# Kernel optimization log

Measured on AMD Instinct MI355X. Metric: run time of the kernel, lower is better.

Reference implementation:

```python
import jax, jax.numpy as jnp
import numpy as np

UNITS = 1024
D_MODEL = 1024
H = 16
DK = 64
DV = 64
M = 128
B = 4
S = 1024


def setup_inputs() -> dict:
    key = jax.random.key(0)
    ks = jax.random.split(key, 12)
    s = 1.0 / np.sqrt(D_MODEL)
    inp = {
        "queries": jax.random.normal(ks[0], (B, S, D_MODEL), jnp.float32),
        "keys": jax.random.normal(ks[1], (B, S, D_MODEL), jnp.float32),
        "values": jax.random.normal(ks[2], (B, S, D_MODEL), jnp.float32),
        "Wq": jax.random.normal(ks[3], (D_MODEL, H * DK), jnp.float32) * s,
        "bq": jnp.zeros((H * DK,), jnp.float32),
        "Wk": jax.random.normal(ks[4], (D_MODEL, H * DK), jnp.float32) * s,
        "bk": jnp.zeros((H * DK,), jnp.float32),
        "Wv": jax.random.normal(ks[5], (D_MODEL, H * DV), jnp.float32) * s,
        "bv": jnp.zeros((H * DV,), jnp.float32),
        "Wo": jax.random.normal(ks[6], (H * DV, UNITS), jnp.float32) * (1.0 / np.sqrt(H * DV)),
        "bo": jnp.zeros((UNITS,), jnp.float32),
        "mk": jax.random.normal(ks[7], (1, M, H * DK), jnp.float32) * 0.1,
        "mv": jax.random.normal(ks[8], (1, M, H * DV), jnp.float32) * 0.1,
        "h": H,
    }
    return inp


def reference(queries, keys, values, Wq, bq, Wk, bk, Wv, bv, Wo, bo, mk, mv, h):
    Bq, Sq, _ = queries.shape
    m = mk.shape[1]
    dk = Wk.shape[1] // h
    dv = Wv.shape[1] // h
    scale_m = jnp.sqrt(jnp.asarray(m, queries.dtype))

    # Q projection: [B, h, Sq, dk]
    q = (queries @ Wq + bq).reshape(Bq, Sq, h, dk).transpose(0, 2, 1, 3)

    # K/V projections with m learned memory slots concatenated on the seq axis
    k_flat = jnp.concatenate(
        [keys @ Wk + bk, scale_m * jnp.broadcast_to(mk, (Bq, m, h * dk))], axis=1
    )  # [B, Sk+m, h*dk]
    v_flat = jnp.concatenate(
        [values @ Wv + bv, scale_m * jnp.broadcast_to(mv, (Bq, m, h * dv))], axis=1
    )  # [B, Sk+m, h*dv]
    Skm = k_flat.shape[1]
    k = k_flat.reshape(Bq, Skm, h, dk).transpose(0, 2, 1, 3)  # [B, h, Sk+m, dk]
    v = v_flat.reshape(Bq, Skm, h, dv).transpose(0, 2, 1, 3)  # [B, h, Sk+m, dv]

    # Scaled dot-product attention over sequence + memory slots
    scores = jnp.einsum("bhqd,bhkd->bhqk", q, k) / jnp.sqrt(jnp.asarray(dk, q.dtype))
    attn = jax.nn.softmax(scores, axis=-1)  # [B, h, Sq, Sk+m]
    out = jnp.einsum("bhqk,bhkd->bhqd", attn, v)  # [B, h, Sq, dv]
    out = out.transpose(0, 2, 1, 3).reshape(Bq, Sq, h * dv)
    return out @ Wo + bo
```

## Files before the change

kernel.cpp:

```cpp
#include <hip/hip_runtime.h>

typedef __attribute__((ext_vector_type(8))) __bf16 bf16x8;
typedef __attribute__((ext_vector_type(4))) float f32x4;

#define DEVINL __device__ __forceinline__

constexpr int BZ = 4;
constexpr int SEQ = 1024;
constexpr int DMODEL = 1024;
constexpr int NH = 16;
constexpr int HD = 64;
constexpr int MSLOT = 128;
constexpr int NT = BZ * SEQ;
constexpr int SKM = SEQ + MSLOT;
constexpr int VT_LD = BZ * SKM;
constexpr float SCALE_M = 11.313708498984761f;
constexpr float SCEXP = 0.18033688011112042f;
constexpr size_t OF_QIN  = 0;
constexpr size_t OF_KIN  = OF_QIN  + (size_t)NT * DMODEL;
constexpr size_t OF_VIN  = OF_KIN  + (size_t)NT * DMODEL;
constexpr size_t OF_WQT  = OF_VIN  + (size_t)NT * DMODEL;
constexpr size_t OF_WKT  = OF_WQT  + (size_t)DMODEL * DMODEL;
constexpr size_t OF_WVT  = OF_WKT  + (size_t)DMODEL * DMODEL;
constexpr size_t OF_WOT  = OF_WVT  + (size_t)DMODEL * DMODEL;
constexpr size_t OF_QB   = OF_WOT  + (size_t)DMODEL * DMODEL;
constexpr size_t OF_KPR  = OF_QB   + (size_t)NT * DMODEL;
constexpr size_t OF_KMEM = OF_KPR  + (size_t)NT * DMODEL;
constexpr size_t OF_VTG  = OF_KMEM + (size_t)MSLOT * DMODEL;
constexpr size_t OF_AOUT = OF_VTG  + (size_t)DMODEL * VT_LD;

DEVINL unsigned short f2bf(float f) {
  union { float f; unsigned u; } v; v.f = f;
  unsigned r = v.u + 0x7FFF + ((v.u >> 16) & 1);
  return (unsigned short)(r >> 16);
}

#if __has_builtin(__builtin_amdgcn_cvt_pk_bf16_f32)
DEVINL unsigned pack2(float a, float b) {
  auto t = __builtin_amdgcn_cvt_pk_bf16_f32(a, b);
  unsigned r; __builtin_memcpy(&r, &t, 4); return r;
}
#else
DEVINL unsigned pack2(float a, float b) {
  return (unsigned)f2bf(a) | ((unsigned)f2bf(b) << 16);
}
#endif

#if __has_builtin(__builtin_amdgcn_exp2f)
DEVINL float fast_exp2(float x) { return __builtin_amdgcn_exp2f(x); }
#else
DEVINL float fast_exp2(float x) { return exp2f(x); }
#endif

DEVINL f32x4 mfma16(bf16x8 a, bf16x8 b, f32x4 c) {
  return __builtin_amdgcn_mfma_f32_16x16x32_bf16(a, b, c, 0, 0, 0);
}

DEVINL void gload16(const unsigned short* gp, unsigned short* lp) {
  __builtin_amdgcn_global_load_lds(
      (const __attribute__((address_space(1))) unsigned int*)(const void*)gp,
      (__attribute__((address_space(3))) unsigned int*)(void*)lp, 16, 0, 0);
}

__global__ __launch_bounds__(256) void prep_all(
    const float* __restrict__ q, const float* __restrict__ k, const float* __restrict__ v,
    const float* __restrict__ W0, const float* __restrict__ W1,
    const float* __restrict__ W2, const float* __restrict__ W3,
    const float* __restrict__ mk, const float* __restrict__ mv,
    unsigned short* __restrict__ dq, unsigned short* __restrict__ dk,
    unsigned short* __restrict__ dv,
    unsigned short* __restrict__ d0, unsigned short* __restrict__ d1,
    unsigned short* __restrict__ d2, unsigned short* __restrict__ d3,
    unsigned short* __restrict__ Kmm, unsigned short* __restrict__ VtG) {
  __shared__ float t[32][65];
  const int tid = threadIdx.x;
  const int bid = blockIdx.x;
  if (bid < 6144) {
    const int tz = bid >> 11;
    const float* src = (tz == 0) ? q : (tz == 1) ? k : v;
    unsigned short* dst = (tz == 0) ? dq : (tz == 1) ? dk : dv;
    int i = ((bid & 2047) * 256 + tid) * 8;
    float4 v0 = *(const float4*)(src + i);
    float4 v1 = *(const float4*)(src + i + 4);
    union { unsigned u2[4]; uint4 v; } o;
    o.u2[0] = pack2(v0.x, v0.y); o.u2[1] = pack2(v0.z, v0.w);
    o.u2[2] = pack2(v1.x, v1.y); o.u2[3] = pack2(v1.z, v1.w);
    *(uint4*)(dst + i) = o.v;
  } else if (bid < 8192) {
    const int rel = bid - 6144;
    const int z = rel >> 9, rem = rel & 511;
    const float* src = (z == 0) ? W0 : (z == 1) ? W1 : (z == 2) ? W2 : W3;
    unsigned short* dst = (z == 0) ? d0 : (z == 1) ? d1 : (z == 2) ? d2 : d3;
    const int n0 = (rem & 31) * 32, k0 = (rem >> 5) * 64;
    {
      int c = tid & 31, rg = tid >> 5;
#pragma unroll
      for (int rr = 0; rr < 8; ++rr)
        t[c][rg * 8 + rr] = src[(size_t)(k0 + rg * 8 + rr) * DMODEL + n0 + c];
    }
    __syncthreads();
    {
      int n = tid >> 3, ck = tid & 7;
      union { unsigned short u[8]; uint4 v; } o;
#pragma unroll
      for (int j = 0; j < 8; ++j) o.u[j] = f2bf(t[n][ck * 8 + j]);
      *(uint4*)(dst + (size_t)(n0 + n) * DMODEL + k0 + ck * 8) = o.v;
    }
  } else if (bid < 8704) {
    int i = (bid - 8192) * 256 + tid;
    Kmm[i] = f2bf(mk[i] * SCALE_M);
  } else {
    const int rel = bid - 8704;
    const int j0 = (rel & 3) * 32, c0 = (rel >> 2) * 32;
    const int tx = tid & 31, ty = tid >> 5;
#pragma unroll
    for (int r = 0; r < 4; ++r)
      t[ty + r * 8][tx] = mv[(size_t)(j0 + ty + r * 8) * DMODEL + c0 + tx];
    __syncthreads();
#pragma unroll
    for (int r = 0; r < 4; ++r) {
      int c = c0 + ty + r * 8;
      unsigned short vv = f2bf(t[tx][ty + r * 8] * SCALE_M);
#pragma unroll
      for (int bb = 0; bb < BZ; ++bb)
        VtG[(size_t)c * VT_LD + bb * SKM + SEQ + j0 + tx] = vv;
    }
  }
}


DEVINL void gemm_stage(const unsigned short* big, const unsigned short* sm,
                       unsigned short* B0, unsigned short* B1,
                       unsigned short* S0, unsigned short* S1,
                       int k0, int tid) {
#pragma unroll
  for (int hb = 0; hb < 2; ++hb) {
    unsigned short* bl = hb ? B1 : B0;
#pragma unroll
    for (int gi = 0; gi < 2; ++gi) {
      int g = gi * 256 + tid;
      int row = g >> 2, slot = g & 3;
      gload16(big + (size_t)row * DMODEL + k0 + hb * 32 + slot * 8, bl + g * 8);
    }
    unsigned short* sl = hb ? S1 : S0;
    int row = tid >> 2, slot = tid & 3;
    gload16(sm + (size_t)row * DMODEL + k0 + hb * 32 + slot * 8, sl + tid * 8);
  }
}

DEVINL void gemm_compute(const unsigned short* B0, const unsigned short* B1,
                         const unsigned short* S0, const unsigned short* S1,
                         int wr, int wc, int quad, int l16, f32x4 acc[4][2]) {
#pragma unroll
  for (int hb = 0; hb < 2; ++hb) {
    const unsigned short* bl = hb ? B1 : B0;
    const unsigned short* sl = hb ? S1 : S0;
    bf16x8 af[4], bfr[2];
#pragma unroll
    for (int rb = 0; rb < 4; ++rb)
      af[rb] = *(const bf16x8*)(bl + (wr * 64 + rb * 16 + l16) * 32 + quad * 8);
#pragma unroll
    for (int cb = 0; cb < 2; ++cb)
      bfr[cb] = *(const bf16x8*)(sl + (wc * 32 + cb * 16 + l16) * 32 + quad * 8);
#pragma unroll
    for (int rb = 0; rb < 4; ++rb)
#pragma unroll
      for (int cb = 0; cb < 2; ++cb)
        acc[rb][cb] = mfma16(af[rb], bfr[cb], acc[rb][cb]);
  }
}

__global__ __launch_bounds__(256) void proj_qkv(
    const unsigned short* __restrict__ Qin, const unsigned short* __restrict__ Kin,
    const unsigned short* __restrict__ Vin, const unsigned short* __restrict__ Wqt,
    const unsigned short* __restrict__ Wkt, const unsigned short* __restrict__ Wvt,
    const float* __restrict__ bq, const float* __restrict__ bk,
    const float* __restrict__ bv, unsigned short* __restrict__ Qbp,
    unsigned short* __restrict__ Kprp, unsigned short* __restrict__ VtG) {
  __shared__ unsigned short Big0[128 * 32], Big1[128 * 32];
  __shared__ unsigned short Sm0[64 * 32], Sm1[64 * 32];
  const int tid = threadIdx.x;
  const int pid = blockIdx.x >> 9;
  const int idx = blockIdx.x & 511;
  const int w = tid >> 6, lane = tid & 63, quad = lane >> 4, l16 = lane & 15;
  const int wr = w >> 1, wc = w & 1;
  f32x4 acc[4][2] = {};

  if (pid < 2) {
    const unsigned short* A  = pid ? Kin : Qin;
    const unsigned short* Wt = pid ? Wkt : Wqt;
    const float* bias        = pid ? bk : bq;
    unsigned short* out      = pid ? Kprp : Qbp;
    const int n0 = (idx & 15) * 64, m0 = (idx >> 4) * 128;
    const unsigned short* big = A + (size_t)m0 * DMODEL;
    const unsigned short* sm  = Wt + (size_t)n0 * DMODEL;
    for (int kt = 0; kt < 16; ++kt) {
      gemm_stage(big, sm, Big0, Big1, Sm0, Sm1, kt * 64, tid);
      __syncthreads();
      gemm_compute(Big0, Big1, Sm0, Sm1, wr, wc, quad, l16, acc);
      __syncthreads();
    }
#pragma unroll
    for (int rb = 0; rb < 4; ++rb)
#pragma unroll
      for (int cb = 0; cb < 2; ++cb)
#pragma unroll
        for (int r = 0; r < 4; ++r) {
          int row = m0 + wr * 64 + rb * 16 + quad * 4 + r;
          int col = n0 + wc * 32 + cb * 16 + l16;
          out[(size_t)row * DMODEL + col] = f2bf(acc[rb][cb][r] + bias[col]);
        }
  } else {
    const int t0 = (idx & 63) * 64, n0 = (idx >> 6) * 128;
    const unsigned short* big = Wvt + (size_t)n0 * DMODEL;
    const unsigned short* sm  = Vin + (size_t)t0 * DMODEL;
    for (int kt = 0; kt < 16; ++kt) {
      gemm_stage(big, sm, Big0, Big1, Sm0, Sm1, kt * 64, tid);
      __syncthreads();
      gemm_compute(Big0, Big1, Sm0, Sm1, wr, wc, quad, l16, acc);
      __syncthreads();
    }
#pragma unroll
    for (int rb = 0; rb < 4; ++rb)
#pragma unroll
      for (int cb = 0; cb < 2; ++cb)
#pragma unroll
        for (int r = 0; r < 4; ++r) {
          int n = n0 + wr * 64 + rb * 16 + quad * 4 + r;
          int tok = t0 + wc * 32 + cb * 16 + l16;
          int col = tok + (tok >> 10) * MSLOT;
          VtG[(size_t)n * VT_LD + col] = f2bf(acc[rb][cb][r] + bv[n]);
        }
  }
}

__global__ __launch_bounds__(256) void gemm_out(const unsigned short* __restrict__ A,
                                                const unsigned short* __restrict__ Wt,
                                                const float* __restrict__ bias,
                                                float* __restrict__ Cout) {
  __shared__ unsigned short Big0[128 * 32], Big1[128 * 32];
  __shared__ unsigned short Sm0[64 * 32], Sm1[64 * 32];
  const int tid = threadIdx.x;
  const int idx = blockIdx.x;
  const int n0 = (idx & 15) * 64, m0 = (idx >> 4) * 128;
  const int w = tid >> 6, lane = tid & 63, quad = lane >> 4, l16 = lane & 15;
  const int wr = w >> 1, wc = w & 1;
  f32x4 acc[4][2] = {};
  const unsigned short* big = A + (size_t)m0 * DMODEL;
  const unsigned short* sm  = Wt + (size_t)n0 * DMODEL;
  for (int kt = 0; kt < 16; ++kt) {
    gemm_stage(big, sm, Big0, Big1, Sm0, Sm1, kt * 64, tid);
    __syncthreads();
    gemm_compute(Big0, Big1, Sm0, Sm1, wr, wc, quad, l16, acc);
    __syncthreads();
  }
#pragma unroll
  for (int rb = 0; rb < 4; ++rb)
#pragma unroll
    for (int cb = 0; cb < 2; ++cb)
#pragma unroll
      for (int r = 0; r < 4; ++r) {
        int row = m0 + wr * 64 + rb * 16 + quad * 4 + r;
        int col = n0 + wc * 32 + cb * 16 + l16;
        Cout[(size_t)row * DMODEL + col] = acc[rb][cb][r] + bias[col];
      }
}

__global__ __launch_bounds__(256) void attn_kernel(const unsigned short* __restrict__ Qb,
                                                   const unsigned short* __restrict__ Kproj,
                                                   const unsigned short* __restrict__ Kmem,
                                                   const unsigned short* __restrict__ VtG,
                                                   unsigned short* __restrict__ Aout) {
  __shared__ unsigned short Ks[64 * 72];
  __shared__ unsigned short Vs[64 * 72];
  __shared__ unsigned short Pl[4 * 32 * 72];
  const int tid = threadIdx.x;
  const int bh = blockIdx.x & 63, qb = blockIdx.x >> 6;
  const int b = bh & 3, h = bh >> 2;
  const int w = tid >> 6, lane = tid & 63, quad = lane >> 4, l16 = lane & 15;
  const int token0 = b * SEQ + qb * 128 + w * 32;
  unsigned short* Pw = Pl + w * 32 * 72;

  const int row0 = tid >> 3, slot0 = tid & 7;
  const int g1 = tid + 256;
  const int row1 = g1 >> 3, slot1 = g1 & 7;

  auto kbase = [&](int tile) -> const unsigned short* {
    return (tile < 16) ? Kproj + (size_t)(b * SEQ + tile * 64) * DMODEL + h * HD
                       : Kmem + (size_t)((tile - 16) * 64) * DMODEL + h * HD;
  };
  auto vbase = [&](int tile) -> const unsigned short* {
    int c0 = (tile < 16) ? b * SKM + tile * 64 : b * SKM + SEQ + (tile - 16) * 64;
    return VtG + (size_t)(h * HD) * VT_LD + c0;
  };

  bf16x8 qf[2][2];
#pragma unroll
  for (int g = 0; g < 2; ++g)
#pragma unroll
    for (int t = 0; t < 2; ++t)
      qf[g][t] = *(const bf16x8*)(Qb + (size_t)(token0 + g * 16 + l16) * DMODEL +
                                  h * HD + t * 32 + quad * 8);

  f32x4 O[2][4] = {};
  float lsum[2] = {0.0f, 0.0f};

  uint4 kr0, kr1, vr0, vr1;
  {
    const unsigned short* kp = kbase(0);
    const unsigned short* vp = vbase(0);
    kr0 = *(const uint4*)(kp + (size_t)row0 * DMODEL + slot0 * 8);
    kr1 = *(const uint4*)(kp + (size_t)row1 * DMODEL + slot1 * 8);
    vr0 = *(const uint4*)(vp + (size_t)row0 * VT_LD + slot0 * 8);
    vr1 = *(const uint4*)(vp + (size_t)row1 * VT_LD + slot1 * 8);
  }

  for (int tile = 0; tile < 18; ++tile) {
    *(uint4*)(Ks + row0 * 72 + slot0 * 8) = kr0;
    *(uint4*)(Ks + row1 * 72 + slot1 * 8) = kr1;
    *(uint4*)(Vs + row0 * 72 + slot0 * 8) = vr0;
    *(uint4*)(Vs + row1 * 72 + slot1 * 8) = vr1;
    __syncthreads();
    if (tile < 17) {
      const unsigned short* kp = kbase(tile + 1);
      const unsigned short* vp = vbase(tile + 1);
      kr0 = *(const uint4*)(kp + (size_t)row0 * DMODEL + slot0 * 8);
      kr1 = *(const uint4*)(kp + (size_t)row1 * DMODEL + slot1 * 8);
      vr0 = *(const uint4*)(vp + (size_t)row0 * VT_LD + slot0 * 8);
      vr1 = *(const uint4*)(vp + (size_t)row1 * VT_LD + slot1 * 8);
    }

#pragma unroll
    for (int g = 0; g < 2; ++g) {
      f32x4 sc[4] = {};
#pragma unroll
      for (int c = 0; c < 4; ++c)
#pragma unroll
        for (int t = 0; t < 2; ++t) {
          bf16x8 kb = *(const bf16x8*)(Ks + (c * 16 + l16) * 72 + t * 32 + quad * 8);
          sc[c] = mfma16(kb, qf[g][t], sc[c]);
        }
#pragma unroll
      for (int c = 0; c < 4; ++c) {
        float p0 = fast_exp2(sc[c][0] * SCEXP);
        float p1 = fast_exp2(sc[c][1] * SCEXP);
        float p2 = fast_exp2(sc[c][2] * SCEXP);
        float p3 = fast_exp2(sc[c][3] * SCEXP);
        lsum[g] += (p0 + p1) + (p2 + p3);
        union { unsigned u[2]; } pk;
        pk.u[0] = pack2(p0, p1);
        pk.u[1] = pack2(p2, p3);
        *(uint2*)(Pw + (g * 16 + l16) * 72 + c * 16 + quad * 4) = *(uint2*)pk.u;
      }
    }
    __builtin_amdgcn_wave_barrier();

#pragma unroll
    for (int t2 = 0; t2 < 2; ++t2) {
      bf16x8 pa0 = *(const bf16x8*)(Pw + (0 + l16) * 72 + t2 * 32 + quad * 8);
      bf16x8 pa1 = *(const bf16x8*)(Pw + (16 + l16) * 72 + t2 * 32 + quad * 8);
#pragma unroll
      for (int c2 = 0; c2 < 4; ++c2) {
        bf16x8 vb = *(const bf16x8*)(Vs + (c2 * 16 + l16) * 72 + t2 * 32 + quad * 8);
        O[0][c2] = mfma16(pa0, vb, O[0][c2]);
        O[1][c2] = mfma16(pa1, vb, O[1][c2]);
      }
    }
    __syncthreads();
  }

#pragma unroll
  for (int g = 0; g < 2; ++g) {
    float ls = lsum[g];
    ls += __shfl_xor(ls, 16);
    ls += __shfl_xor(ls, 32);
#pragma unroll
    for (int r = 0; r < 4; ++r) {
      float lv = __shfl(ls, quad * 4 + r, 16);
      float inv = 1.0f / lv;
#pragma unroll
      for (int c2 = 0; c2 < 4; ++c2)
        Aout[(size_t)(token0 + g * 16 + quad * 4 + r) * DMODEL + h * HD + c2 * 16 + l16] =
            f2bf(O[g][c2][r] * inv);
    }
  }
}

extern "C" void kernel_launch(void* const* d_in, const int* in_sizes, int n_in,
                              void* d_out, int out_size, void* d_ws, size_t ws_size,
                              hipStream_t stream) {
  const float* queries = (const float*)d_in[0];
  const float* keys    = (const float*)d_in[1];
  const float* values  = (const float*)d_in[2];
  const float* Wq = (const float*)d_in[3];
  const float* bq = (const float*)d_in[4];
  const float* Wk = (const float*)d_in[5];
  const float* bk = (const float*)d_in[6];
  const float* Wv = (const float*)d_in[7];
  const float* bv = (const float*)d_in[8];
  const float* Wo = (const float*)d_in[9];
  const float* bo = (const float*)d_in[10];
  const float* mk = (const float*)d_in[11];
  const float* mv = (const float*)d_in[12];

  unsigned short* ws = (unsigned short*)d_ws;
  unsigned short* Qin  = ws + OF_QIN;
  unsigned short* Kin  = ws + OF_KIN;
  unsigned short* Vin  = ws + OF_VIN;
  unsigned short* Wqt  = ws + OF_WQT;
  unsigned short* Wkt  = ws + OF_WKT;
  unsigned short* Wvt  = ws + OF_WVT;
  unsigned short* Wot  = ws + OF_WOT;
  unsigned short* Qbp  = ws + OF_QB;
  unsigned short* Kprp = ws + OF_KPR;
  unsigned short* Kmm  = ws + OF_KMEM;
  unsigned short* VtGp = ws + OF_VTG;
  unsigned short* Aoutp = ws + OF_AOUT;

  prep_all<<<8832, 256, 0, stream>>>(queries, keys, values, Wq, Wk, Wv, Wo, mk, mv,
                                     Qin, Kin, Vin, Wqt, Wkt, Wvt, Wot, Kmm, VtGp);

  proj_qkv<<<1536, 256, 0, stream>>>(Qin, Kin, Vin, Wqt, Wkt, Wvt, bq, bk, bv,
                                     Qbp, Kprp, VtGp);

  attn_kernel<<<512, 256, 0, stream>>>(Qbp, Kprp, Kmm, VtGp, Aoutp);

  gemm_out<<<512, 256, 0, stream>>>(Aoutp, Wot, bo, (float*)d_out);
}
```

Before: 222.2 us.

## Halve attention query tile to double block count; reorder GEMM block index mapping

The attention kernel now assigns 16 query rows per wave (64 per block) instead of 32, which doubles the grid to 1024 blocks and halves per-wave registers and P scratch in shared memory. This aims at better occupancy and CU load balance across the device. The cost is that each K/V tile staged into shared memory now serves half as many queries, so global K/V traffic doubles. Separately, the Q/K projection and output GEMMs swap their block-index mapping so consecutive blocks walk along M rather than N, which changes which A and W tiles are in L2 at the same time.

```diff
diff --git a/kernel.cpp b/kernel.cpp
--- a/kernel.cpp
+++ b/kernel.cpp
@@ -191,7 +191,7 @@
     const unsigned short* Wt = pid ? Wkt : Wqt;
     const float* bias        = pid ? bk : bq;
     unsigned short* out      = pid ? Kprp : Qbp;
-    const int n0 = (idx & 15) * 64, m0 = (idx >> 4) * 128;
+    const int m0 = (idx & 31) * 128, n0 = (idx >> 5) * 64;
     const unsigned short* big = A + (size_t)m0 * DMODEL;
     const unsigned short* sm  = Wt + (size_t)n0 * DMODEL;
     for (int kt = 0; kt < 16; ++kt) {
@@ -242,7 +242,7 @@
   __shared__ unsigned short Sm0[64 * 32], Sm1[64 * 32];
   const int tid = threadIdx.x;
   const int idx = blockIdx.x;
-  const int n0 = (idx & 15) * 64, m0 = (idx >> 4) * 128;
+  const int m0 = (idx & 31) * 128, n0 = (idx >> 5) * 64;
   const int w = tid >> 6, lane = tid & 63, quad = lane >> 4, l16 = lane & 15;
   const int wr = w >> 1, wc = w & 1;
   f32x4 acc[4][2] = {};
@@ -273,13 +273,13 @@
                                                    unsigned short* __restrict__ Aout) {
   __shared__ unsigned short Ks[64 * 72];
   __shared__ unsigned short Vs[64 * 72];
-  __shared__ unsigned short Pl[4 * 32 * 72];
+  __shared__ unsigned short Pl[4 * 16 * 72];
   const int tid = threadIdx.x;
   const int bh = blockIdx.x & 63, qb = blockIdx.x >> 6;
   const int b = bh & 3, h = bh >> 2;
   const int w = tid >> 6, lane = tid & 63, quad = lane >> 4, l16 = lane & 15;
-  const int token0 = b * SEQ + qb * 128 + w * 32;
-  unsigned short* Pw = Pl + w * 32 * 72;
+  const int token0 = b * SEQ + qb * 64 + w * 16;
+  unsigned short* Pw = Pl + w * 16 * 72;
 
   const int row0 = tid >> 3, slot0 = tid & 7;
   const int g1 = tid + 256;
@@ -294,16 +294,13 @@
     return VtG + (size_t)(h * HD) * VT_LD + c0;
   };
 
-  bf16x8 qf[2][2];
-#pragma unroll
-  for (int g = 0; g < 2; ++g)
-#pragma unroll
-    for (int t = 0; t < 2; ++t)
-      qf[g][t] = *(const bf16x8*)(Qb + (size_t)(token0 + g * 16 + l16) * DMODEL +
-                                  h * HD + t * 32 + quad * 8);
-
-  f32x4 O[2][4] = {};
-  float lsum[2] = {0.0f, 0.0f};
+  bf16x8 qf[2];
+#pragma unroll
+  for (int t = 0; t < 2; ++t)
+    qf[t] = *(const bf16x8*)(Qb + (size_t)(token0 + l16) * DMODEL + h * HD + t * 32 + quad * 8);
+
+  f32x4 O[4] = {};
+  float lsum = 0.0f;
 
   uint4 kr0, kr1, vr0, vr1;
   {
@@ -330,59 +327,51 @@
       vr1 = *(const uint4*)(vp + (size_t)row1 * VT_LD + slot1 * 8);
     }
 
-#pragma unroll
-    for (int g = 0; g < 2; ++g) {
-      f32x4 sc[4] = {};
-#pragma unroll
-      for (int c = 0; c < 4; ++c)
-#pragma unroll
-        for (int t = 0; t < 2; ++t) {
-          bf16x8 kb = *(const bf16x8*)(Ks + (c * 16 + l16) * 72 + t * 32 + quad * 8);
-          sc[c] = mfma16(kb, qf[g][t], sc[c]);
-        }
-#pragma unroll
-      for (int c = 0; c < 4; ++c) {
-        float p0 = fast_exp2(sc[c][0] * SCEXP);
-        float p1 = fast_exp2(sc[c][1] * SCEXP);
-        float p2 = fast_exp2(sc[c][2] * SCEXP);
-        float p3 = fast_exp2(sc[c][3] * SCEXP);
-        lsum[g] += (p0 + p1) + (p2 + p3);
-        union { unsigned u[2]; } pk;
-        pk.u[0] = pack2(p0, p1);
-        pk.u[1] = pack2(p2, p3);
-        *(uint2*)(Pw + (g * 16 + l16) * 72 + c * 16 + quad * 4) = *(uint2*)pk.u;
+    f32x4 sc[4] = {};
+#pragma unroll
+    for (int c = 0; c < 4; ++c)
+#pragma unroll
+      for (int t = 0; t < 2; ++t) {
+        bf16x8 kb = *(const bf16x8*)(Ks + (c * 16 + l16) * 72 + t * 32 + quad * 8);
+        sc[c] = mfma16(kb, qf[t], sc[c]);
       }
+
+#pragma unroll
+    for (int c = 0; c < 4; ++c) {
+      float p0 = fast_exp2(sc[c][0] * SCEXP);
+      float p1 = fast_exp2(sc[c][1] * SCEXP);
+      float p2 = fast_exp2(sc[c][2] * SCEXP);
+      float p3 = fast_exp2(sc[c][3] * SCEXP);
+      lsum += (p0 + p1) + (p2 + p3);
+      union { unsigned u[2]; } pk;
+      pk.u[0] = pack2(p0, p1);
+      pk.u[1] = pack2(p2, p3);
+      *(uint2*)(Pw + l16 * 72 + c * 16 + quad * 4) = *(uint2*)pk.u;
     }
     __builtin_amdgcn_wave_barrier();
 
 #pragma unroll
     for (int t2 = 0; t2 < 2; ++t2) {
-      bf16x8 pa0 = *(const bf16x8*)(Pw + (0 + l16) * 72 + t2 * 32 + quad * 8);
-      bf16x8 pa1 = *(const bf16x8*)(Pw + (16 + l16) * 72 + t2 * 32 + quad * 8);
+      bf16x8 pa = *(const bf16x8*)(Pw + l16 * 72 + t2 * 32 + quad * 8);
 #pragma unroll
       for (int c2 = 0; c2 < 4; ++c2) {
         bf16x8 vb = *(const bf16x8*)(Vs + (c2 * 16 + l16) * 72 + t2 * 32 + quad * 8);
-        O[0][c2] = mfma16(pa0, vb, O[0][c2]);
-        O[1][c2] = mfma16(pa1, vb, O[1][c2]);
+        O[c2] = mfma16(pa, vb, O[c2]);
       }
     }
     __syncthreads();
   }
 
-#pragma unroll
-  for (int g = 0; g < 2; ++g) {
-    float ls = lsum[g];
-    ls += __shfl_xor(ls, 16);
-    ls += __shfl_xor(ls, 32);
-#pragma unroll
-    for (int r = 0; r < 4; ++r) {
-      float lv = __shfl(ls, quad * 4 + r, 16);
-      float inv = 1.0f / lv;
-#pragma unroll
-      for (int c2 = 0; c2 < 4; ++c2)
-        Aout[(size_t)(token0 + g * 16 + quad * 4 + r) * DMODEL + h * HD + c2 * 16 + l16] =
-            f2bf(O[g][c2][r] * inv);
-    }
+  lsum += __shfl_xor(lsum, 16);
+  lsum += __shfl_xor(lsum, 32);
+#pragma unroll
+  for (int r = 0; r < 4; ++r) {
+    float lv = __shfl(lsum, quad * 4 + r, 16);
+    float inv = 1.0f / lv;
+#pragma unroll
+    for (int c2 = 0; c2 < 4; ++c2)
+      Aout[(size_t)(token0 + quad * 4 + r) * DMODEL + h * HD + c2 * 16 + l16] =
+          f2bf(O[c2][r] * inv);
   }
 }
 
@@ -423,7 +412,7 @@
   proj_qkv<<<1536, 256, 0, stream>>>(Qin, Kin, Vin, Wqt, Wkt, Wvt, bq, bk, bv,
                                      Qbp, Kprp, VtGp);
 
-  attn_kernel<<<512, 256, 0, stream>>>(Qbp, Kprp, Kmm, VtGp, Aoutp);
+  attn_kernel<<<1024, 256, 0, stream>>>(Qbp, Kprp, Kmm, VtGp, Aoutp);
 
   gemm_out<<<512, 256, 0, stream>>>(Aoutp, Wot, bo, (float*)d_out);
 }
```

New measurement: 217.9 us. No clear change (-2.0%).
